# Performance work log

Measured on AMD Instinct MI355X. Metric: run time of the kernel, lower is better.

The kernel has to match this reference:

```python
import jax, jax.numpy as jnp
import numpy as np

EPS = 1e-6

def setup_inputs() -> dict:
    key = jax.random.key(0)
    ks = jax.random.split(key, 8)
    B, S, E, C = 2, 2048, 1024, 256
    x = jax.random.normal(ks[0], (B, S, E), dtype=jnp.float32)
    mask = jnp.triu(jnp.ones((S, S), dtype=bool), k=1)  # True = masked (causal)
    conditioning = jax.random.normal(ks[1], (B, C), dtype=jnp.float32)
    sc = 1.0 / np.sqrt(E)
    Wq = jax.random.normal(ks[2], (E, E), dtype=jnp.float32) * sc
    Wk = jax.random.normal(ks[3], (E, E), dtype=jnp.float32) * sc
    Wv = jax.random.normal(ks[4], (E, E), dtype=jnp.float32) * sc
    Wo = jax.random.normal(ks[5], (E, E), dtype=jnp.float32) * sc
    rms_scale = jnp.ones((E,), dtype=jnp.float32)
    Wc = jax.random.normal(ks[6], (2 * E, C), dtype=jnp.float32) * 0.02
    bc = jax.random.normal(ks[7], (2 * E,), dtype=jnp.float32) * 0.02
    return {"x": x, "mask": mask, "conditioning": conditioning,
            "Wq": Wq, "Wk": Wk, "Wv": Wv, "Wo": Wo,
            "rms_scale": rms_scale, "Wc": Wc, "bc": bc}

def reference(x, mask, conditioning, Wq, Wk, Wv, Wo, rms_scale, Wc, bc):
    B, S, E = x.shape
    H = 16
    D = E // H
    scale = D ** -0.5
    # QKV projections (nn.Linear: x @ W.T), reshape to (B,H,S,D)
    def proj(W):
        return (x @ W.T).reshape(B, S, H, D).transpose(0, 2, 1, 3)
    q, k, v = proj(Wq), proj(Wk), proj(Wv)
    # attention scores (B,H,S,S)
    scores = jnp.einsum('bhsd,bhtd->bhst', q, k) * scale
    scores = jnp.where(mask[None, None, :, :], -jnp.inf, scores)
    attn = jax.nn.softmax(scores, axis=-1)
    out = jnp.einsum('bhst,bhtd->bhsd', attn, v)  # (B,H,S,D)
    out = out.transpose(0, 2, 1, 3).reshape(B, S, E)
    out = out @ Wo.T
    # AdaptiveRMSNorm + FiLM
    rms = jnp.sqrt(jnp.mean(out * out, axis=-1, keepdims=True) + EPS)
    xn = out / rms * rms_scale
    mod = jax.nn.silu(conditioning) @ Wc.T + bc  # (B, 2E)
    shift, sc = jnp.split(mod, 2, axis=-1)
    xn = xn * (1.0 + sc[:, None, :]) + shift[:, None, :]
    return xn
```

## Files before the change

kernel.cpp:

```cpp
#include <hip/hip_runtime.h>
#include <hip/hip_bf16.h>
#include <stdint.h>

typedef __bf16 bf16;
typedef __bf16 bf16x4 __attribute__((ext_vector_type(4)));
typedef __bf16 bf16x8 __attribute__((ext_vector_type(8)));
typedef float  f32x4  __attribute__((ext_vector_type(4)));

#define NB 2
#define NS 2048
#define NE 1024
#define NH 16
#define ND 64
#define NC 256

#define EXP2(x) __builtin_amdgcn_exp2f(x)

__device__ __forceinline__ void gload16(void* lds, const void* g) {
  __builtin_amdgcn_global_load_lds(
      (const __attribute__((address_space(1))) void*)g,
      (__attribute__((address_space(3))) void*)lds, 16, 0, 0);
}

__global__ __launch_bounds__(256) void cvt_all_kernel(
    const float* __restrict__ x,  const float* __restrict__ w0,
    const float* __restrict__ w1, const float* __restrict__ w2,
    const float* __restrict__ w3, bf16* __restrict__ xb,
    bf16* __restrict__ wb,
    const float* __restrict__ cond, const float* __restrict__ Wc,
    const float* __restrict__ bc, float* __restrict__ mod) {
  int blk = blockIdx.x;
  if (blk >= 4096) {
    __shared__ float scond[NC];
    int mb = blk - 4096;
    int b  = mb >> 3;
    int j0 = (mb & 7) * 256;
    float c = cond[b * NC + threadIdx.x];
    scond[threadIdx.x] = c / (1.f + __expf(-c));
    __syncthreads();
    int j = j0 + threadIdx.x;
    float acc = bc[j];
    const float* wrow = Wc + (size_t)j * NC;
    for (int cc = 0; cc < NC; ++cc) acc += scond[cc] * wrow[cc];
    mod[b * 2 * NE + j] = acc;
    return;
  }
  const float* s; bf16* d; int off;
  if (blk < 2048) {
    s = x; d = xb; off = blk * 2048;
  } else {
    int seg = (blk - 2048) >> 9, bb = (blk - 2048) & 511;
    const float* ws[4] = {w0, w1, w2, w3};
    s = ws[seg]; d = wb + seg * 1048576; off = bb * 2048;
  }
  int i = off + threadIdx.x * 8;
  float4 a = ((const float4*)(s + i))[0];
  float4 b = ((const float4*)(s + i))[1];
  bf16x8 o;
  o[0] = (bf16)a.x; o[1] = (bf16)a.y; o[2] = (bf16)a.z; o[3] = (bf16)a.w;
  o[4] = (bf16)b.x; o[5] = (bf16)b.y; o[6] = (bf16)b.z; o[7] = (bf16)b.w;
  *(bf16x8*)(d + i) = o;
}

template<int MODE>
__global__ __launch_bounds__(256) void gemm128(
    const bf16* __restrict__ A, const bf16* __restrict__ W0,
    const bf16* __restrict__ W1, const bf16* __restrict__ W2,
    void* __restrict__ out, int K) {
  __shared__ bf16 As[128 * 32];
  __shared__ bf16 Bs[128 * 32];
  const int t = threadIdx.x, w = t >> 6, l = t & 63;
  const int lr = l & 15, lg = l >> 4;
  const int wm = w >> 1, wn = w & 1;
  const int m0 = blockIdx.x * 128;
  const int ng = blockIdx.y * 128;

  const bf16* Bw;
  if (MODE == 0) {
    const bf16* Ws[3] = {W0, W1, W2};
    Bw = Ws[ng >> 10] + (size_t)(ng & 1023) * K;
  } else {
    Bw = W0 + (size_t)ng * K;
  }

  f32x4 acc[4][4];
#pragma unroll
  for (int i = 0; i < 4; ++i)
#pragma unroll
    for (int j = 0; j < 4; ++j) acc[i][j] = (f32x4){0.f, 0.f, 0.f, 0.f};

  const int srow = (l >> 2);
  const int scol = (l & 3) * 8;

  for (int kt = 0; kt < K; kt += 32) {
#pragma unroll
    for (int r = 0; r < 2; ++r) {
      int cc = w * 2 + r;
      int row = cc * 16 + srow;
      gload16((char*)As + cc * 1024, A  + (size_t)(m0 + row) * K + kt + scol);
      gload16((char*)Bs + cc * 1024, Bw + (size_t)row        * K + kt + scol);
    }
    __syncthreads();
    bf16x8 af[4], bfr[4];
#pragma unroll
    for (int i = 0; i < 4; ++i) {
      af[i]  = *(const bf16x8*)(As + (wm * 64 + i * 16 + lr) * 32 + lg * 8);
      bfr[i] = *(const bf16x8*)(Bs + (wn * 64 + i * 16 + lr) * 32 + lg * 8);
    }
#pragma unroll
    for (int i = 0; i < 4; ++i)
#pragma unroll
      for (int j = 0; j < 4; ++j)
        acc[i][j] = __builtin_amdgcn_mfma_f32_16x16x32_bf16(af[i], bfr[j], acc[i][j], 0, 0, 0);
    if (kt + 32 < K) __syncthreads();
  }

#pragma unroll
  for (int i = 0; i < 4; ++i) {
#pragma unroll
    for (int j = 0; j < 4; ++j) {
#pragma unroll
      for (int r = 0; r < 4; ++r) {
        int row = m0 + wm * 64 + i * 16 + lg * 4 + r;
        int col = ng + wn * 64 + j * 16 + lr;
        float v = acc[i][j][r];
        if (MODE == 1) {
          ((bf16*)out)[(size_t)row * NE + col] = (bf16)v;
        } else {
          int b = row >> 11, s = row & 2047;
          int wi = col >> 10, nc = col & 1023;
          int h = nc >> 6, d = nc & 63;
          size_t hb = (size_t)(b * NH + h) * 131072u;
          size_t idx;
          if (wi == 0) v *= 0.180336880f;
          if (wi == 2)
            idx = 8388608u + hb +
                  (size_t)((d >> 4) * 32768 + (s >> 3) * 128 + (d & 15) * 8 + (s & 7));
          else
            idx = (size_t)wi * 4194304u + hb +
                  (size_t)((s >> 4) * 1024 + (d >> 3) * 128 + (s & 15) * 8 + (d & 7));
          ((bf16*)out)[idx] = (bf16)v;
        }
      }
    }
  }
}

__global__ __launch_bounds__(256, 4) void attn_kernel(
    const bf16* __restrict__ Q, const bf16* __restrict__ Km,
    const bf16* __restrict__ Vt, bf16* __restrict__ O) {
  __shared__ float smrg[4][24][64];
  const int l = threadIdx.x & 63, w = threadIdx.x >> 6;
  const int lr = l & 15, lg = l >> 4;
  const int bid = blockIdx.x;
  const int xcd = bid & 7, slot = bid >> 3;
  const int bh = xcd * 4 + (slot >> 5);
  const int b = bh >> 4, h = bh & 15;
  const int sl = slot & 31;
  const int tp = sl * 2 + (w >> 1);
  const int hw = w & 1;

  bf16* pb = (bf16*)&smrg[w][0][0];

  const bf16* Qh = Q  + (size_t)bh * 131072u + l * 8;
  const bf16* Kh = Km + (size_t)bh * 131072u + l * 8;
  const bf16* Vh = Vt + (size_t)bh * 131072u + l * 8;

  bf16x8 ones;
#pragma unroll
  for (int i = 0; i < 8; ++i) ones[i] = (bf16)1.0f;

  for (int pass = 0; pass < 2; ++pass) {
    const int qbase = (pass ? (127 - tp) : tp) * 16;

    bf16x8 qf0 = *(const bf16x8*)(Qh + (qbase >> 4) * 1024);
    bf16x8 qf1 = *(const bf16x8*)(Qh + (qbase >> 4) * 1024 + 512);

    f32x4 o[4], osum;
#pragma unroll
    for (int dt = 0; dt < 4; ++dt) o[dt] = (f32x4){0.f, 0.f, 0.f, 0.f};
    osum = (f32x4){0.f, 0.f, 0.f, 0.f};
    int qr[4];
#pragma unroll
    for (int r = 0; r < 4; ++r) qr[r] = qbase + lg * 4 + r;

    for (int kv0 = hw * 64; kv0 < qbase + 16; kv0 += 128) {
      const bf16* kt = Kh + (kv0 >> 4) * 1024;
      const bf16* vt = Vh + (kv0 >> 3) * 128;
      bf16x8 k0[4], k1[4], v0[4], v1[4];
#pragma unroll
      for (int nt = 0; nt < 4; ++nt) {
        k0[nt] = *(const bf16x8*)(kt + nt * 1024);
        k1[nt] = *(const bf16x8*)(kt + nt * 1024 + 512);
      }
#pragma unroll
      for (int dt = 0; dt < 4; ++dt) {
        v0[dt] = *(const bf16x8*)(vt + dt * 32768);
        v1[dt] = *(const bf16x8*)(vt + dt * 32768 + 512);
      }
      f32x4 s[4];
#pragma unroll
      for (int nt = 0; nt < 4; ++nt) {
        f32x4 z = (f32x4){0.f, 0.f, 0.f, 0.f};
        z = __builtin_amdgcn_mfma_f32_16x16x32_bf16(qf0, k0[nt], z, 0, 0, 0);
        z = __builtin_amdgcn_mfma_f32_16x16x32_bf16(qf1, k1[nt], z, 0, 0, 0);
        s[nt] = z;
      }
      const bool edge = (kv0 + 63 > qbase);
#pragma unroll
      for (int nt = 0; nt < 4; ++nt) {
#pragma unroll
        for (int r = 0; r < 4; ++r) {
          float sv = s[nt][r];
          if (edge && (kv0 + nt * 16 + lr > qr[r])) sv = -1e30f;
          pb[(lg * 4 + r) * 72 + nt * 16 + lr] = (bf16)EXP2(sv);
        }
      }
      asm volatile("s_waitcnt lgkmcnt(0)" ::: "memory");
      __builtin_amdgcn_sched_barrier(0);
      bf16x8 pa0 = *(const bf16x8*)(pb + lr * 72 + lg * 8);
      bf16x8 pa1 = *(const bf16x8*)(pb + lr * 72 + 32 + lg * 8);
      osum = __builtin_amdgcn_mfma_f32_16x16x32_bf16(pa0, ones, osum, 0, 0, 0);
      osum = __builtin_amdgcn_mfma_f32_16x16x32_bf16(pa1, ones, osum, 0, 0, 0);
#pragma unroll
      for (int dt = 0; dt < 4; ++dt) {
        o[dt] = __builtin_amdgcn_mfma_f32_16x16x32_bf16(pa0, v0[dt], o[dt], 0, 0, 0);
        o[dt] = __builtin_amdgcn_mfma_f32_16x16x32_bf16(pa1, v1[dt], o[dt], 0, 0, 0);
      }
    }

    float* my = &smrg[w][0][0];
#pragma unroll
    for (int r = 0; r < 4; ++r) my[(4 + r) * 64 + l] = osum[r];
#pragma unroll
    for (int dt = 0; dt < 4; ++dt)
#pragma unroll
      for (int r = 0; r < 4; ++r) my[(8 + dt * 4 + r) * 64 + l] = o[dt][r];
    __syncthreads();

    const float* pt = &smrg[w ^ 1][0][0];
    float rl[4];
#pragma unroll
    for (int r = 0; r < 4; ++r)
      rl[r] = 1.f / (osum[r] + pt[(4 + r) * 64 + l]);
#pragma unroll
    for (int dd = 0; dd < 2; ++dd) {
      const int dt = hw * 2 + dd;
#pragma unroll
      for (int r = 0; r < 4; ++r) {
        float val = o[dt][r] + pt[(8 + dt * 4 + r) * 64 + l];
        O[((size_t)(b * NS) + qr[r]) * NE + h * ND + dt * 16 + lr] =
            (bf16)(val * rl[r]);
      }
    }
    __syncthreads();
  }
}

__global__ __launch_bounds__(256) void norm_kernel(
    const bf16* __restrict__ tmp, const float* __restrict__ rms_scale,
    const float* __restrict__ mod, float* __restrict__ out) {
  int row = blockIdx.x;
  int b = row >> 11;
  const bf16* trow = tmp + (size_t)row * NE;
  bf16x4 v = ((const bf16x4*)trow)[threadIdx.x];
  float vv[4] = {(float)v[0], (float)v[1], (float)v[2], (float)v[3]};
  float ss = vv[0]*vv[0] + vv[1]*vv[1] + vv[2]*vv[2] + vv[3]*vv[3];
#pragma unroll
  for (int mk = 1; mk < 64; mk <<= 1) ss += __shfl_xor(ss, mk, 64);
  __shared__ float sred[4];
  if ((threadIdx.x & 63) == 0) sred[threadIdx.x >> 6] = ss;
  __syncthreads();
  float tot = sred[0] + sred[1] + sred[2] + sred[3];
  float rinv = rsqrtf(tot * (1.f / NE) + 1e-6f);
  const float* modb = mod + b * 2 * NE;
#pragma unroll
  for (int j = 0; j < 4; ++j) {
    int e = threadIdx.x * 4 + j;
    float xn = vv[j] * rinv * rms_scale[e];
    xn = xn * (1.f + modb[NE + e]) + modb[e];
    out[(size_t)row * NE + e] = xn;
  }
}

extern "C" void kernel_launch(void* const* d_in, const int* in_sizes, int n_in,
                              void* d_out, int out_size, void* d_ws, size_t ws_size,
                              hipStream_t stream) {
  const float* x    = (const float*)d_in[0];
  const float* cond = (const float*)d_in[2];
  const float* Wq   = (const float*)d_in[3];
  const float* Wk   = (const float*)d_in[4];
  const float* Wv   = (const float*)d_in[5];
  const float* Wo   = (const float*)d_in[6];
  const float* rmss = (const float*)d_in[7];
  const float* Wc   = (const float*)d_in[8];
  const float* bc   = (const float*)d_in[9];
  float* out = (float*)d_out;

  char* ws = (char*)d_ws;
  const size_t MB = 1u << 20;
  bf16*  xb  = (bf16*)(ws);
  bf16*  Wqb = (bf16*)(ws + 8  * MB);
  bf16*  Wob = (bf16*)(ws + 14 * MB);
  bf16*  Qb  = (bf16*)(ws + 16 * MB);
  bf16*  Kb  = (bf16*)(ws + 24 * MB);
  bf16*  Vt  = (bf16*)(ws + 32 * MB);
  bf16*  Oa  = (bf16*)(ws);
  bf16*  tmp = (bf16*)(ws + 16 * MB);
  float* mod = (float*)(ws + 40 * MB);

  cvt_all_kernel<<<4112, 256, 0, stream>>>(x, Wq, Wk, Wv, Wo, xb, Wqb,
                                           cond, Wc, bc, mod);

  gemm128<0><<<dim3(32, 24), 256, 0, stream>>>(xb, Wqb, Wqb + 1048576, Wqb + 2097152, Qb, NE);

  attn_kernel<<<1024, 256, 0, stream>>>(Qb, Kb, Vt, Oa);

  gemm128<1><<<dim3(32, 8), 256, 0, stream>>>(Oa, Wob, nullptr, nullptr, tmp, NE);

  norm_kernel<<<NB * NS, 256, 0, stream>>>(tmp, rmss, mod, out);
}
```

Measured before the change: 127.2 us.

## Split output-projection GEMM into 64-row tiles and peel causal edge block in attention

The output-projection GEMM gets its own kernel with 64x128 tiles, doubling the grid from 256 to 512 blocks so more CUs are occupied on this small GEMM. The cost is less reuse of each loaded tile. In attention, the main KV loop now covers only fully unmasked 64-wide blocks with no mask check, and the diagonal block is peeled into a separate masked section. This removes per-element compare and select work from the inner loop but duplicates code and may raise register pressure.

Result: faster. 123.4 us (-3.0%).

```diff
diff --git a/kernel.cpp b/kernel.cpp
--- a/kernel.cpp
+++ b/kernel.cpp
@@ -62,11 +62,10 @@
   *(bf16x8*)(d + i) = o;
 }
 
-template<int MODE>
-__global__ __launch_bounds__(256) void gemm128(
+__global__ __launch_bounds__(256) void gemm_qkv(
     const bf16* __restrict__ A, const bf16* __restrict__ W0,
     const bf16* __restrict__ W1, const bf16* __restrict__ W2,
-    void* __restrict__ out, int K) {
+    bf16* __restrict__ out, int K) {
   __shared__ bf16 As[128 * 32];
   __shared__ bf16 Bs[128 * 32];
   const int t = threadIdx.x, w = t >> 6, l = t & 63;
@@ -75,13 +74,8 @@
   const int m0 = blockIdx.x * 128;
   const int ng = blockIdx.y * 128;
 
-  const bf16* Bw;
-  if (MODE == 0) {
-    const bf16* Ws[3] = {W0, W1, W2};
-    Bw = Ws[ng >> 10] + (size_t)(ng & 1023) * K;
-  } else {
-    Bw = W0 + (size_t)ng * K;
-  }
+  const bf16* Ws[3] = {W0, W1, W2};
+  const bf16* Bw = Ws[ng >> 10] + (size_t)(ng & 1023) * K;
 
   f32x4 acc[4][4];
 #pragma unroll
@@ -124,26 +118,84 @@
         int row = m0 + wm * 64 + i * 16 + lg * 4 + r;
         int col = ng + wn * 64 + j * 16 + lr;
         float v = acc[i][j][r];
-        if (MODE == 1) {
-          ((bf16*)out)[(size_t)row * NE + col] = (bf16)v;
-        } else {
-          int b = row >> 11, s = row & 2047;
-          int wi = col >> 10, nc = col & 1023;
-          int h = nc >> 6, d = nc & 63;
-          size_t hb = (size_t)(b * NH + h) * 131072u;
-          size_t idx;
-          if (wi == 0) v *= 0.180336880f;
-          if (wi == 2)
-            idx = 8388608u + hb +
-                  (size_t)((d >> 4) * 32768 + (s >> 3) * 128 + (d & 15) * 8 + (s & 7));
-          else
-            idx = (size_t)wi * 4194304u + hb +
-                  (size_t)((s >> 4) * 1024 + (d >> 3) * 128 + (s & 15) * 8 + (d & 7));
-          ((bf16*)out)[idx] = (bf16)v;
-        }
-      }
-    }
-  }
+        int b = row >> 11, s = row & 2047;
+        int wi = col >> 10, nc = col & 1023;
+        int h = nc >> 6, d = nc & 63;
+        size_t hb = (size_t)(b * NH + h) * 131072u;
+        size_t idx;
+        if (wi == 0) v *= 0.180336880f;
+        if (wi == 2)
+          idx = 8388608u + hb +
+                (size_t)((d >> 4) * 32768 + (s >> 3) * 128 + (d & 15) * 8 + (s & 7));
+        else
+          idx = (size_t)wi * 4194304u + hb +
+                (size_t)((s >> 4) * 1024 + (d >> 3) * 128 + (s & 15) * 8 + (d & 7));
+        out[idx] = (bf16)v;
+      }
+    }
+  }
+}
+
+__global__ __launch_bounds__(256) void gemm_op(
+    const bf16* __restrict__ A, const bf16* __restrict__ Bw,
+    bf16* __restrict__ out) {
+  __shared__ bf16 As[64 * 32];
+  __shared__ bf16 Bs[128 * 32];
+  const int t = threadIdx.x, w = t >> 6, l = t & 63;
+  const int lr = l & 15, lg = l >> 4;
+  const int wm = w >> 1, wn = w & 1;
+  const int m0 = blockIdx.x * 64;
+  const int n0 = blockIdx.y * 128;
+  const int K = NE;
+
+  f32x4 acc[2][4];
+#pragma unroll
+  for (int i = 0; i < 2; ++i)
+#pragma unroll
+    for (int j = 0; j < 4; ++j) acc[i][j] = (f32x4){0.f, 0.f, 0.f, 0.f};
+
+  const int srow = (l >> 2);
+  const int scol = (l & 3) * 8;
+
+  for (int kt = 0; kt < K; kt += 32) {
+#pragma unroll
+    for (int r = 0; r < 3; ++r) {
+      int cc = w * 3 + r;
+      if (cc < 4) {
+        gload16((char*)As + cc * 1024,
+                A + (size_t)(m0 + cc * 16 + srow) * K + kt + scol);
+      } else {
+        int cb = cc - 4;
+        gload16((char*)Bs + cb * 1024,
+                Bw + (size_t)(n0 + cb * 16 + srow) * K + kt + scol);
+      }
+    }
+    __syncthreads();
+    bf16x8 af[2], bfr[4];
+#pragma unroll
+    for (int i = 0; i < 2; ++i)
+      af[i] = *(const bf16x8*)(As + (wm * 32 + i * 16 + lr) * 32 + lg * 8);
+#pragma unroll
+    for (int j = 0; j < 4; ++j)
+      bfr[j] = *(const bf16x8*)(Bs + (wn * 64 + j * 16 + lr) * 32 + lg * 8);
+#pragma unroll
+    for (int i = 0; i < 2; ++i)
+#pragma unroll
+      for (int j = 0; j < 4; ++j)
+        acc[i][j] = __builtin_amdgcn_mfma_f32_16x16x32_bf16(af[i], bfr[j], acc[i][j], 0, 0, 0);
+    if (kt + 32 < K) __syncthreads();
+  }
+
+#pragma unroll
+  for (int i = 0; i < 2; ++i)
+#pragma unroll
+    for (int j = 0; j < 4; ++j)
+#pragma unroll
+      for (int r = 0; r < 4; ++r) {
+        int row = m0 + wm * 32 + i * 16 + lg * 4 + r;
+        int col = n0 + wn * 64 + j * 16 + lr;
+        out[(size_t)row * NE + col] = (bf16)acc[i][j][r];
+      }
 }
 
 __global__ __launch_bounds__(256, 4) void attn_kernel(
@@ -180,11 +232,10 @@
 #pragma unroll
     for (int dt = 0; dt < 4; ++dt) o[dt] = (f32x4){0.f, 0.f, 0.f, 0.f};
     osum = (f32x4){0.f, 0.f, 0.f, 0.f};
-    int qr[4];
-#pragma unroll
-    for (int r = 0; r < 4; ++r) qr[r] = qbase + lg * 4 + r;
-
-    for (int kv0 = hw * 64; kv0 < qbase + 16; kv0 += 128) {
+
+    const int kv_edge = qbase & ~63;
+
+    for (int kv0 = hw * 64; kv0 < kv_edge; kv0 += 128) {
       const bf16* kt = Kh + (kv0 >> 4) * 1024;
       const bf16* vt = Vh + (kv0 >> 3) * 128;
       bf16x8 k0[4], k1[4], v0[4], v1[4];
@@ -206,16 +257,11 @@
         z = __builtin_amdgcn_mfma_f32_16x16x32_bf16(qf1, k1[nt], z, 0, 0, 0);
         s[nt] = z;
       }
-      const bool edge = (kv0 + 63 > qbase);
-#pragma unroll
-      for (int nt = 0; nt < 4; ++nt) {
-#pragma unroll
-        for (int r = 0; r < 4; ++r) {
-          float sv = s[nt][r];
-          if (edge && (kv0 + nt * 16 + lr > qr[r])) sv = -1e30f;
-          pb[(lg * 4 + r) * 72 + nt * 16 + lr] = (bf16)EXP2(sv);
-        }
-      }
+#pragma unroll
+      for (int nt = 0; nt < 4; ++nt)
+#pragma unroll
+        for (int r = 0; r < 4; ++r)
+          pb[(lg * 4 + r) * 72 + nt * 16 + lr] = (bf16)EXP2(s[nt][r]);
       asm volatile("s_waitcnt lgkmcnt(0)" ::: "memory");
       __builtin_amdgcn_sched_barrier(0);
       bf16x8 pa0 = *(const bf16x8*)(pb + lr * 72 + lg * 8);
@@ -229,6 +275,53 @@
       }
     }
 
+    if (((kv_edge >> 6) & 1) == hw) {
+      const int kv0 = kv_edge;
+      const bf16* kt = Kh + (kv0 >> 4) * 1024;
+      const bf16* vt = Vh + (kv0 >> 3) * 128;
+      bf16x8 k0[4], k1[4], v0[4], v1[4];
+#pragma unroll
+      for (int nt = 0; nt < 4; ++nt) {
+        k0[nt] = *(const bf16x8*)(kt + nt * 1024);
+        k1[nt] = *(const bf16x8*)(kt + nt * 1024 + 512);
+      }
+#pragma unroll
+      for (int dt = 0; dt < 4; ++dt) {
+        v0[dt] = *(const bf16x8*)(vt + dt * 32768);
+        v1[dt] = *(const bf16x8*)(vt + dt * 32768 + 512);
+      }
+      f32x4 s[4];
+#pragma unroll
+      for (int nt = 0; nt < 4; ++nt) {
+        f32x4 z = (f32x4){0.f, 0.f, 0.f, 0.f};
+        z = __builtin_amdgcn_mfma_f32_16x16x32_bf16(qf0, k0[nt], z, 0, 0, 0);
+        z = __builtin_amdgcn_mfma_f32_16x16x32_bf16(qf1, k1[nt], z, 0, 0, 0);
+        s[nt] = z;
+      }
+      int qr[4];
+#pragma unroll
+      for (int r = 0; r < 4; ++r) qr[r] = qbase + lg * 4 + r;
+#pragma unroll
+      for (int nt = 0; nt < 4; ++nt)
+#pragma unroll
+        for (int r = 0; r < 4; ++r) {
+          float sv = s[nt][r];
+          if (kv0 + nt * 16 + lr > qr[r]) sv = -1e30f;
+          pb[(lg * 4 + r) * 72 + nt * 16 + lr] = (bf16)EXP2(sv);
+        }
+      asm volatile("s_waitcnt lgkmcnt(0)" ::: "memory");
+      __builtin_amdgcn_sched_barrier(0);
+      bf16x8 pa0 = *(const bf16x8*)(pb + lr * 72 + lg * 8);
+      bf16x8 pa1 = *(const bf16x8*)(pb + lr * 72 + 32 + lg * 8);
+      osum = __builtin_amdgcn_mfma_f32_16x16x32_bf16(pa0, ones, osum, 0, 0, 0);
+      osum = __builtin_amdgcn_mfma_f32_16x16x32_bf16(pa1, ones, osum, 0, 0, 0);
+#pragma unroll
+      for (int dt = 0; dt < 4; ++dt) {
+        o[dt] = __builtin_amdgcn_mfma_f32_16x16x32_bf16(pa0, v0[dt], o[dt], 0, 0, 0);
+        o[dt] = __builtin_amdgcn_mfma_f32_16x16x32_bf16(pa1, v1[dt], o[dt], 0, 0, 0);
+      }
+    }
+
     float* my = &smrg[w][0][0];
 #pragma unroll
     for (int r = 0; r < 4; ++r) my[(4 + r) * 64 + l] = osum[r];
@@ -249,7 +342,7 @@
 #pragma unroll
       for (int r = 0; r < 4; ++r) {
         float val = o[dt][r] + pt[(8 + dt * 4 + r) * 64 + l];
-        O[((size_t)(b * NS) + qr[r]) * NE + h * ND + dt * 16 + lr] =
+        O[((size_t)(b * NS) + qbase + lg * 4 + r) * NE + h * ND + dt * 16 + lr] =
             (bf16)(val * rl[r]);
       }
     }
@@ -312,11 +405,11 @@
   cvt_all_kernel<<<4112, 256, 0, stream>>>(x, Wq, Wk, Wv, Wo, xb, Wqb,
                                            cond, Wc, bc, mod);
 
-  gemm128<0><<<dim3(32, 24), 256, 0, stream>>>(xb, Wqb, Wqb + 1048576, Wqb + 2097152, Qb, NE);
+  gemm_qkv<<<dim3(32, 24), 256, 0, stream>>>(xb, Wqb, Wqb + 1048576, Wqb + 2097152, Qb, NE);
 
   attn_kernel<<<1024, 256, 0, stream>>>(Qb, Kb, Vt, Oa);
 
-  gemm128<1><<<dim3(32, 8), 256, 0, stream>>>(Oa, Wob, nullptr, nullptr, tmp, NE);
+  gemm_op<<<dim3(64, 8), 256, 0, stream>>>(Oa, Wob, tmp);
 
   norm_kernel<<<NB * NS, 256, 0, stream>>>(tmp, rmss, mod, out);
 }
```
